# Optimization experiments

Measured on AMD Instinct MI355X. Metric: run time of the kernel, lower is better.

Reference implementation:

```python
import math
import jax, jax.numpy as jnp
import numpy as np

NUM_HEAD = 16

def get_slopes(n):
    def pow2(n):
        start = 2 ** (-(2 ** (-(math.log2(n) - 3))))
        return [start * start ** i for i in range(n)]
    if math.log2(n).is_integer():
        return pow2(n)
    c = 2 ** math.floor(math.log2(n))
    return pow2(c) + get_slopes(2 * c)[0::2][: n - c]

def setup_inputs() -> dict:
    key = jax.random.key(0)
    ks = jax.random.split(key, 5)
    B, T, D = 2, 2048, 1024
    x = jax.random.normal(ks[0], (B, T, D), dtype=jnp.float32)
    Wq = jax.random.normal(ks[1], (D, D), dtype=jnp.float32) * 0.02
    Wk = jax.random.normal(ks[2], (D, D), dtype=jnp.float32) * 0.02
    Wv = jax.random.normal(ks[3], (D, D), dtype=jnp.float32) * 0.02
    Wo = jax.random.normal(ks[4], (D, D), dtype=jnp.float32) * (0.02 / math.sqrt(2 * 24))
    return {"x": x, "Wq": Wq, "Wk": Wk, "Wv": Wv, "Wo": Wo}

def reference(x, Wq, Wk, Wv, Wo):
    B, T, D = x.shape
    H = NUM_HEAD
    hd = D // H
    # projections (no bias)
    q = (x @ Wq).reshape(B, T, H, hd).transpose(0, 2, 1, 3)  # b h t d
    k = (x @ Wk).reshape(B, T, H, hd).transpose(0, 2, 1, 3)
    v = (x @ Wv).reshape(B, T, H, hd).transpose(0, 2, 1, 3)
    scores = jnp.einsum("bhqd,bhkd->bhqk", q, k) / jnp.sqrt(jnp.asarray(hd, dtype=q.dtype))
    # ALiBi bias: slopes[h] * (j - (T-1)), broadcast over query positions
    slopes = jnp.asarray(np.array(get_slopes(H), dtype=np.float32))
    alibi = slopes[:, None, None] * (jnp.arange(T, dtype=jnp.float32) - (T - 1))[None, None, :]  # h 1 k
    scores = scores + alibi[None]  # b h q k
    causal = jnp.tril(jnp.ones((T, T), dtype=bool))
    masked = jnp.where(causal[None, None], scores.astype(jnp.float32), jnp.finfo(jnp.float32).min)
    p = jax.nn.softmax(masked, axis=-1)
    attn_out = jnp.einsum("bhqk,bhkd->bhqd", p, v)
    attn_out = attn_out.transpose(0, 2, 1, 3).reshape(B, T, D)
    return attn_out @ Wo
```

## Files before the change

kernel.cpp:

```cpp
#include <hip/hip_runtime.h>
#include <hip/hip_bf16.h>
#include <math.h>

#define B_ 2
#define T_ 2048
#define D_ 1024
#define H_ 16
#define HD 64

typedef __bf16 bf16;
typedef bf16 bf16x8 __attribute__((ext_vector_type(8)));
typedef bf16 bf16x4 __attribute__((ext_vector_type(4)));
typedef short short4v __attribute__((ext_vector_type(4)));
typedef float f32x4 __attribute__((ext_vector_type(4)));

#define GL2LDS16(g, l) __builtin_amdgcn_global_load_lds(                      \
    (const __attribute__((address_space(1))) void*)(g),                       \
    (__attribute__((address_space(3))) void*)(l), 16, 0, 0)

static __device__ __forceinline__ f32x4 mfma16x16x16(bf16x4 a, bf16x4 b, f32x4 c) {
#if defined(__HIP_DEVICE_COMPILE__)
# if __has_builtin(__builtin_amdgcn_mfma_f32_16x16x16bf16_1k)
    return __builtin_amdgcn_mfma_f32_16x16x16bf16_1k(
        __builtin_bit_cast(short4v, a), __builtin_bit_cast(short4v, b), c, 0, 0, 0);
# else
    asm("v_mfma_f32_16x16x16_bf16 %0, %1, %2, %0" : "+v"(c) : "v"(a), "v"(b));
    return c;
# endif
#else
    (void)a; (void)b;
    return c;
#endif
}

static __device__ __forceinline__ bf16x4 lo4(bf16x8 v) {
    return __builtin_shufflevector(v, v, 0, 1, 2, 3);
}
static __device__ __forceinline__ bf16x4 hi4(bf16x8 v) {
    return __builtin_shufflevector(v, v, 4, 5, 6, 7);
}

__global__ __launch_bounds__(256) void prep_inputs(const float* __restrict__ x,
                                                   const float* __restrict__ W0,
                                                   const float* __restrict__ W1,
                                                   const float* __restrict__ W2,
                                                   const float* __restrict__ W3,
                                                   bf16* __restrict__ xb,
                                                   bf16* __restrict__ Wt) {
    const int z = blockIdx.z;
    const int tid = threadIdx.x;
    if (z >= 4) {
        size_t i = ((((size_t)(z - 4) * 256 + blockIdx.y * 16 + blockIdx.x) * 256) + tid) * 4;
        float4 v = *(const float4*)(x + i);
        bf16 tmp[4] = {(bf16)v.x, (bf16)v.y, (bf16)v.z, (bf16)v.w};
        *(uint2*)(xb + i) = *(const uint2*)tmp;
        return;
    }
    __shared__ bf16 tile[64 * 72];
    const float* W = (z == 0) ? W0 : (z == 1) ? W1 : (z == 2) ? W2 : W3;
    bf16* out = Wt + (size_t)z * D_ * D_;
    const int k0 = blockIdx.y * 64, n0 = blockIdx.x * 64;
    for (int it = 0; it < 4; ++it) {
        int idx = it * 256 + tid;
        int r = idx >> 4;
        int c4 = (idx & 15) << 2;
        float4 v = *(const float4*)(W + (size_t)(k0 + r) * D_ + n0 + c4);
        tile[(c4 + 0) * 72 + r] = (bf16)v.x;
        tile[(c4 + 1) * 72 + r] = (bf16)v.y;
        tile[(c4 + 2) * 72 + r] = (bf16)v.z;
        tile[(c4 + 3) * 72 + r] = (bf16)v.w;
    }
    __syncthreads();
    for (int it = 0; it < 2; ++it) {
        int idx = it * 256 + tid;
        int r = idx >> 3;
        int c8 = (idx & 7) << 3;
        bf16x8 v = *(const bf16x8*)&tile[r * 72 + c8];
        *(bf16x8*)(out + (size_t)(n0 + r) * D_ + k0 + c8) = v;
    }
}

__global__ __launch_bounds__(256) void gemm_qkv(const bf16* __restrict__ A,
                                                const bf16* __restrict__ Bt,
                                                bf16* __restrict__ Cout) {
    __shared__ bf16 As[2][2][128 * 32];
    __shared__ bf16 Bs[2][3][2][64 * 32];
    const int bid = blockIdx.x;
    const int xcd = bid & 7, rr = bid >> 3;
    const int y   = (xcd << 2) + (rr & 3);
    const int xx  = rr >> 2;
    const int m0 = y * 128, n0 = xx * 64;

    const int tid = threadIdx.x;
    const int wave = tid >> 6, lane = tid & 63;
    const int quad = lane >> 4, l16 = lane & 15;
    const int wr = wave >> 1, wc = wave & 1;

    const int lrow = lane >> 2, lcol = (lane & 3) << 3;
    const bf16* ag = A + (size_t)(m0 + wave * 32 + lrow) * D_ + lcol;
    const size_t brow = (size_t)(n0 + wave * 16 + lrow) * D_ + lcol;
    const int a_off = (wave * 32 + lrow) * 32 + lcol;
    const int b_off = (wave * 16 + lrow) * 32 + lcol;

    f32x4 acc[3][4][2];
#pragma unroll
    for (int z = 0; z < 3; ++z)
#pragma unroll
        for (int mi = 0; mi < 4; ++mi)
#pragma unroll
            for (int ni = 0; ni < 2; ++ni) acc[z][mi][ni] = (f32x4){0.f, 0.f, 0.f, 0.f};

    auto stage = [&](int buf, int kb) {
        GL2LDS16(ag + kb,                        &As[buf][0][a_off]);
        GL2LDS16(ag + (size_t)16 * D_ + kb,      &As[buf][0][a_off + 16 * 32]);
        GL2LDS16(ag + kb + 32,                   &As[buf][1][a_off]);
        GL2LDS16(ag + (size_t)16 * D_ + kb + 32, &As[buf][1][a_off + 16 * 32]);
#pragma unroll
        for (int z = 0; z < 3; ++z) {
            const bf16* bg = Bt + (size_t)z * D_ * D_ + brow;
            GL2LDS16(bg + kb,      &Bs[buf][z][0][b_off]);
            GL2LDS16(bg + kb + 32, &Bs[buf][z][1][b_off]);
        }
    };

    stage(0, 0);
    __syncthreads();
    int cur = 0;
    for (int kb = 0; kb < D_; kb += 64) {
        if (kb + 64 < D_) stage(cur ^ 1, kb + 64);
#pragma unroll
        for (int half = 0; half < 2; ++half) {
            bf16x8 af[4];
#pragma unroll
            for (int mi = 0; mi < 4; ++mi)
                af[mi] = *(const bf16x8*)&As[cur][half][(wr * 64 + mi * 16 + l16) * 32 + quad * 8];
#pragma unroll
            for (int z = 0; z < 3; ++z) {
                bf16x8 bfr[2];
#pragma unroll
                for (int ni = 0; ni < 2; ++ni)
                    bfr[ni] = *(const bf16x8*)&Bs[cur][z][half][(wc * 32 + ni * 16 + l16) * 32 + quad * 8];
                if (z < 2) {
#pragma unroll
                    for (int mi = 0; mi < 4; ++mi)
#pragma unroll
                        for (int ni = 0; ni < 2; ++ni)
                            acc[z][mi][ni] = __builtin_amdgcn_mfma_f32_16x16x32_bf16(
                                bfr[ni], af[mi], acc[z][mi][ni], 0, 0, 0);
                } else {
#pragma unroll
                    for (int mi = 0; mi < 4; ++mi)
#pragma unroll
                        for (int ni = 0; ni < 2; ++ni)
                            acc[z][mi][ni] = __builtin_amdgcn_mfma_f32_16x16x32_bf16(
                                af[mi], bfr[ni], acc[z][mi][ni], 0, 0, 0);
                }
            }
        }
        __syncthreads();
        cur ^= 1;
    }

#pragma unroll
    for (int z = 0; z < 3; ++z) {
        bf16* Cb = Cout + (size_t)z * (B_ * T_) * D_;
        const float qscale = (z == 0) ? 0.180336887f : 1.0f;
        if (z < 2) {
#pragma unroll
            for (int mi = 0; mi < 4; ++mi)
#pragma unroll
                for (int ni = 0; ni < 2; ++ni) {
                    int m = m0 + wr * 64 + mi * 16 + l16;
                    int n = n0 + wc * 32 + ni * 16 + quad * 4;
                    int b = m >> 11, t = m & (T_ - 1);
                    int h = n >> 6, d = n & (HD - 1);
                    bf16 o4[4];
                    for (int r = 0; r < 4; ++r) o4[r] = (bf16)(acc[z][mi][ni][r] * qscale);
                    *(uint2*)&Cb[(((((size_t)b * H_ + h) * T_ + t) << 6) + d)] =
                        *(const uint2*)o4;
                }
        } else {
#pragma unroll
            for (int mi = 0; mi < 4; ++mi)
#pragma unroll
                for (int ni = 0; ni < 2; ++ni) {
                    int m = m0 + wr * 64 + mi * 16 + quad * 4;
                    int n = n0 + wc * 32 + ni * 16 + l16;
                    int b = m >> 11, t = m & (T_ - 1);
                    int h = n >> 6, d = n & (HD - 1);
                    bf16 o4[4];
                    for (int r = 0; r < 4; ++r) o4[r] = (bf16)acc[z][mi][ni][r];
                    *(uint2*)&Cb[((((size_t)b * H_ + h) * HD + d) * T_ + t)] =
                        *(const uint2*)o4;
                }
        }
    }
}

__global__ __launch_bounds__(256) void gemm_out(const bf16* __restrict__ A,
                                                const bf16* __restrict__ Bt,
                                                float* __restrict__ Cout) {
    __shared__ bf16 As[2][2][128 * 32];
    __shared__ bf16 Bs[2][2][64 * 32];
    const int bid = blockIdx.x;
    const int xcd = bid & 7, rr = bid >> 3;
    const int y   = (xcd << 2) + (rr & 3);
    const int xx  = rr >> 2;
    const int m0 = y * 128, n0 = xx * 64;

    const int tid = threadIdx.x;
    const int wave = tid >> 6, lane = tid & 63;
    const int quad = lane >> 4, l16 = lane & 15;
    const int wr = wave >> 1, wc = wave & 1;

    const int lrow = lane >> 2, lcol = (lane & 3) << 3;
    const bf16* ag = A  + (size_t)(m0 + wave * 32 + lrow) * D_ + lcol;
    const bf16* bg = Bt + (size_t)(n0 + wave * 16 + lrow) * D_ + lcol;
    const int a_off = (wave * 32 + lrow) * 32 + lcol;
    const int b_off = (wave * 16 + lrow) * 32 + lcol;

    f32x4 acc[4][2];
    for (int mi = 0; mi < 4; ++mi)
        for (int ni = 0; ni < 2; ++ni) acc[mi][ni] = (f32x4){0.f, 0.f, 0.f, 0.f};

    auto stage = [&](int buf, int kb) {
        GL2LDS16(ag + kb,                        &As[buf][0][a_off]);
        GL2LDS16(ag + (size_t)16 * D_ + kb,      &As[buf][0][a_off + 16 * 32]);
        GL2LDS16(ag + kb + 32,                   &As[buf][1][a_off]);
        GL2LDS16(ag + (size_t)16 * D_ + kb + 32, &As[buf][1][a_off + 16 * 32]);
        GL2LDS16(bg + kb,                        &Bs[buf][0][b_off]);
        GL2LDS16(bg + kb + 32,                   &Bs[buf][1][b_off]);
    };

    stage(0, 0);
    __syncthreads();
    int cur = 0;
    for (int kb = 0; kb < D_; kb += 64) {
        if (kb + 64 < D_) stage(cur ^ 1, kb + 64);
#pragma unroll
        for (int half = 0; half < 2; ++half) {
            bf16x8 af[4], bfr[2];
#pragma unroll
            for (int mi = 0; mi < 4; ++mi)
                af[mi] = *(const bf16x8*)&As[cur][half][(wr * 64 + mi * 16 + l16) * 32 + quad * 8];
#pragma unroll
            for (int ni = 0; ni < 2; ++ni)
                bfr[ni] = *(const bf16x8*)&Bs[cur][half][(wc * 32 + ni * 16 + l16) * 32 + quad * 8];
#pragma unroll
            for (int mi = 0; mi < 4; ++mi)
#pragma unroll
                for (int ni = 0; ni < 2; ++ni)
                    acc[mi][ni] = __builtin_amdgcn_mfma_f32_16x16x32_bf16(
                        bfr[ni], af[mi], acc[mi][ni], 0, 0, 0);
        }
        __syncthreads();
        cur ^= 1;
    }

    for (int mi = 0; mi < 4; ++mi)
        for (int ni = 0; ni < 2; ++ni) {
            int m = m0 + wr * 64 + mi * 16 + l16;
            int n = n0 + wc * 32 + ni * 16 + quad * 4;
            *(f32x4*)&Cout[(size_t)m * D_ + n] = acc[mi][ni];
        }
}

__device__ __constant__ unsigned char ITEM_QT[24] = {
    8,9,10,11,12,13,14,15, 7,15, 6,14, 5,13, 4,12, 3,11, 2,10, 1,9, 0,8};
__device__ __constant__ unsigned char ITEM_KIND[24] = {
    1,1,1,1,1,1,1,1, 0,2, 0,2, 0,2, 0,2, 0,2, 0,2, 0,2, 0,2};

#define LDP 136

struct VStage { bf16x8 v0, v1; };

__global__ __launch_bounds__(512, 4) void attn_kernel(const bf16* __restrict__ Q,
                                                      const bf16* __restrict__ K,
                                                      const bf16* __restrict__ Vt,
                                                      bf16* __restrict__ O,
                                                      float* __restrict__ Opart,
                                                      float2* __restrict__ ML) {
    __shared__ bf16 Kh[2][2][128 * 32];
    __shared__ bf16 Vs[64 * LDP];

    const int bh = blockIdx.x;
    const int item = blockIdx.y;
    const int qt = ITEM_QT[item];
    const int kind = ITEM_KIND[item];
    const int h = bh & (H_ - 1), b = bh >> 4;
    const int tid = threadIdx.x;
    const int wave = tid >> 6, lane = tid & 63;
    const int quad = lane >> 4, l16 = lane & 15;

    const bf16* Qb = Q + (size_t)bh * T_ * HD;
    const bf16* Kb = K + (size_t)bh * T_ * HD;
    const bf16* Vb = Vt + (size_t)bh * HD * T_;

    const float slope2 = exp2f(-0.5f * (float)(h + 1)) * 1.44269504f;

    bf16x8 qf[2];
    {
        const bf16* qrow = Qb + (size_t)(qt * 128 + wave * 16 + l16) * HD + quad * 8;
        qf[0] = *(const bf16x8*)(qrow);
        qf[1] = *(const bf16x8*)(qrow + 32);
    }

    auto stageK = [&](int buf, int t) {
        const bf16* kg = Kb + ((size_t)t * 128 + (tid >> 2)) * HD + ((tid & 3) << 3);
        GL2LDS16(kg,      &Kh[buf][0][tid * 8]);
        GL2LDS16(kg + 32, &Kh[buf][1][tid * 8]);
    };

    const int slot0 = tid, slot1 = 512 + tid;
    const int rv0 = slot0 >> 4, c0 = slot0 & 15;
    const int rv1 = slot1 >> 4, c1 = slot1 & 15;
    const int vs0 = rv0 * LDP + (c0 & 1) * 64 + (c0 >> 1) * 4;
    const int vs1 = rv1 * LDP + (c1 & 1) * 64 + (c1 >> 1) * 4;

    auto loadV = [&](int t, VStage& st) {
        const bf16* vb = Vb + t * 128;
        st.v0 = *(const bf16x8*)(vb + (size_t)rv0 * T_ + c0 * 8);
        st.v1 = *(const bf16x8*)(vb + (size_t)rv1 * T_ + c1 * 8);
    };
    auto storeV = [&](const VStage& st) {
        *(bf16x4*)&Vs[vs0]      = lo4(st.v0);
        *(bf16x4*)&Vs[vs0 + 32] = hi4(st.v0);
        *(bf16x4*)&Vs[vs1]      = lo4(st.v1);
        *(bf16x4*)&Vs[vs1 + 32] = hi4(st.v1);
    };

    f32x4 acc[4];
    for (int df = 0; df < 4; ++df) acc[df] = (f32x4){0.f, 0.f, 0.f, 0.f};
    float m_run = -INFINITY, l_lane = 0.f;

    const int qglob = qt * 128 + wave * 16 + l16;
    const int nkt = qt + 1;
    const int kt0 = (kind == 2) ? 8 : 0;
    const int kt1 = (kind == 1) ? 8 : nkt;

    auto compute = [&](int kt, int buf, bool last) {
        f32x4 s[8];
#pragma unroll
        for (int nf = 0; nf < 8; ++nf) {
            bf16x8 kf0 = *(const bf16x8*)&Kh[buf][0][(nf * 16 + l16) * 32 + quad * 8];
            bf16x8 kf1 = *(const bf16x8*)&Kh[buf][1][(nf * 16 + l16) * 32 + quad * 8];
            f32x4 zz = (f32x4){0.f, 0.f, 0.f, 0.f};
            __builtin_amdgcn_s_setprio(1);
            zz = __builtin_amdgcn_mfma_f32_16x16x32_bf16(kf0, qf[0], zz, 0, 0, 0);
            zz = __builtin_amdgcn_mfma_f32_16x16x32_bf16(kf1, qf[1], zz, 0, 0, 0);
            __builtin_amdgcn_s_setprio(0);
            s[nf] = zz;
        }

        const float j0f = (float)(kt * 128 + quad * 4 - (T_ - 1));
#pragma unroll
        for (int nf = 0; nf < 8; ++nf)
#pragma unroll
            for (int r = 0; r < 4; ++r)
                s[nf][r] += slope2 * (j0f + (float)(nf * 16 + r));
        if (last) {
            const int jb = kt * 128 + quad * 4;
#pragma unroll
            for (int nf = 0; nf < 8; ++nf)
#pragma unroll
                for (int r = 0; r < 4; ++r)
                    if (jb + nf * 16 + r > qglob) s[nf][r] = -INFINITY;
        }

        float a[8];
#pragma unroll
        for (int nf = 0; nf < 8; ++nf)
            a[nf] = fmaxf(fmaxf(s[nf][0], s[nf][1]), fmaxf(s[nf][2], s[nf][3]));
        float t0 = fmaxf(a[0], a[1]), t1 = fmaxf(a[2], a[3]);
        float t2 = fmaxf(a[4], a[5]), t3 = fmaxf(a[6], a[7]);
        float mx = fmaxf(fmaxf(t0, t1), fmaxf(t2, t3));
        mx = fmaxf(mx, __shfl_xor(mx, 16, 64));
        mx = fmaxf(mx, __shfl_xor(mx, 32, 64));

        if (!__all(mx - m_run <= 8.f)) {
            const float mnew = fmaxf(m_run, mx);
            const float alpha = exp2f(m_run - mnew);
            l_lane *= alpha;
#pragma unroll
            for (int df = 0; df < 4; ++df) acc[df] *= alpha;
            m_run = mnew;
        }

        float rs0 = 0.f, rs1 = 0.f;
        bf16x4 pf[8];
#pragma unroll
        for (int nf = 0; nf < 8; ++nf) {
            float p0 = exp2f(s[nf][0] - m_run);
            float p1 = exp2f(s[nf][1] - m_run);
            float p2 = exp2f(s[nf][2] - m_run);
            float p3 = exp2f(s[nf][3] - m_run);
            if (nf & 1) rs1 += (p0 + p1) + (p2 + p3);
            else        rs0 += (p0 + p1) + (p2 + p3);
            pf[nf] = (bf16x4){(bf16)p0, (bf16)p1, (bf16)p2, (bf16)p3};
        }
        l_lane += rs0 + rs1;

#pragma unroll
        for (int j = 0; j < 4; ++j) {
            bf16x8 w[4];
#pragma unroll
            for (int df = 0; df < 4; ++df)
                w[df] = *(const bf16x8*)&Vs[(df * 16 + l16) * LDP + quad * 32 + j * 8];
            __builtin_amdgcn_s_setprio(1);
#pragma unroll
            for (int df = 0; df < 4; ++df) {
                acc[df] = mfma16x16x16(lo4(w[df]), pf[2 * j],     acc[df]);
                acc[df] = mfma16x16x16(hi4(w[df]), pf[2 * j + 1], acc[df]);
            }
            __builtin_amdgcn_s_setprio(0);
        }
    };

    VStage sA, sB;
    stageK(0, kt0);
    loadV(kt0, sA);
    int kt = kt0;
    for (;;) {
        __syncthreads();
        storeV(sA);
        __syncthreads();
        if (kt + 1 < kt1) { stageK(1, kt + 1); loadV(kt + 1, sB); }
        compute(kt, 0, kt == nkt - 1);
        if (++kt >= kt1) break;
        __syncthreads();
        storeV(sB);
        __syncthreads();
        if (kt + 1 < kt1) { stageK(0, kt + 1); loadV(kt + 1, sA); }
        compute(kt, 1, kt == nkt - 1);
        if (++kt >= kt1) break;
    }

    float l_run = l_lane;
    l_run += __shfl_xor(l_run, 16, 64);
    l_run += __shfl_xor(l_run, 32, 64);

    if (kind == 0) {
        const float inv = 1.0f / l_run;
        for (int df = 0; df < 4; ++df) {
            bf16 o4[4];
            for (int r = 0; r < 4; ++r) o4[r] = (bf16)(acc[df][r] * inv);
            *(uint2*)&O[(((size_t)b * T_ + qglob) * H_ + h) * HD + df * 16 + quad * 4] =
                *(const uint2*)o4;
        }
    } else {
        const int pidx = (bh * 8 + (qt - 8)) * 2 + (kind == 2 ? 1 : 0);
        const int ql = wave * 16 + l16;
        float* dst = Opart + (size_t)pidx * 8192 + ql * 64;
        for (int df = 0; df < 4; ++df)
            *(f32x4*)&dst[df * 16 + quad * 4] = acc[df];
        if (quad == 0) ML[pidx * 128 + ql] = make_float2(m_run, l_run);
    }
}

__global__ __launch_bounds__(512) void attn_merge(const float* __restrict__ Opart,
                                                  const float2* __restrict__ ML,
                                                  bf16* __restrict__ O) {
    const int qt = 8 + blockIdx.x, bh = blockIdx.y;
    const int h = bh & (H_ - 1), b = bh >> 4;
    const int tid = threadIdx.x;
    const int q = tid >> 2, dc = (tid & 3) << 4;
    const int p0 = (bh * 8 + blockIdx.x) * 2, p1 = p0 + 1;

    const float2 ml0 = ML[p0 * 128 + q], ml1 = ML[p1 * 128 + q];
    const float M = fmaxf(ml0.x, ml1.x);
    const float e0 = exp2f(ml0.x - M), e1 = exp2f(ml1.x - M);
    const float inv = 1.0f / (e0 * ml0.y + e1 * ml1.y);

    const float* a = Opart + (size_t)p0 * 8192 + q * 64 + dc;
    const float* c = Opart + (size_t)p1 * 8192 + q * 64 + dc;
    bf16 o16[16];
    for (int j = 0; j < 4; ++j) {
        f32x4 va = *(const f32x4*)(a + j * 4);
        f32x4 vc = *(const f32x4*)(c + j * 4);
        for (int r = 0; r < 4; ++r)
            o16[j * 4 + r] = (bf16)((va[r] * e0 + vc[r] * e1) * inv);
    }
    const int t = qt * 128 + q;
    bf16* dst = O + (((size_t)b * T_ + t) * H_ + h) * HD + dc;
    *(bf16x8*)dst = *(const bf16x8*)o16;
    *(bf16x8*)(dst + 8) = *(const bf16x8*)(o16 + 8);
}

extern "C" void kernel_launch(void* const* d_in, const int* in_sizes, int n_in,
                              void* d_out, int out_size, void* d_ws, size_t ws_size,
                              hipStream_t stream) {
    const float* x  = (const float*)d_in[0];
    const float* Wq = (const float*)d_in[1];
    const float* Wk = (const float*)d_in[2];
    const float* Wv = (const float*)d_in[3];
    const float* Wo = (const float*)d_in[4];
    float* out = (float*)d_out;

    const size_t M = (size_t)B_ * T_;
    const size_t XE = M * D_;
    const size_t WE = (size_t)D_ * D_;

    char* ws = (char*)d_ws;
    size_t off = 0;
    auto carve = [&](size_t bytes) {
        void* p = ws + off;
        off += (bytes + 255) & ~(size_t)255;
        return p;
    };
    bf16* xb  = (bf16*)carve(XE * 2);
    bf16* Wt  = (bf16*)carve(4 * WE * 2);
    bf16* QKV = (bf16*)carve(3 * XE * 2);
    float*  Opart = (float*)carve(32 * 8 * 2 * 8192 * sizeof(float));
    float2* MLbuf = (float2*)carve(32 * 8 * 2 * 128 * sizeof(float2));
    bf16* attn = xb;

    prep_inputs<<<dim3(16, 16, 20), 256, 0, stream>>>(x, Wq, Wk, Wv, Wo, xb, Wt);

    gemm_qkv<<<512, 256, 0, stream>>>(xb, Wt, QKV);
    attn_kernel<<<dim3(32, 24), 512, 0, stream>>>(QKV, QKV + XE, QKV + 2 * XE,
                                                  attn, Opart, MLbuf);
    attn_merge<<<dim3(8, 32), 512, 0, stream>>>(Opart, MLbuf, attn);
    gemm_out<<<512, 256, 0, stream>>>(attn, Wt + 3 * WE, out);
}
```

Measured before the change: 182.8 us.

## Split causal attention into 4-tile KV chunks with multi-way partial merge

Replaces the two-way split of late query tiles with a finer split where each block handles at most four key tiles, giving 40 work items per head and a merge that combines up to four partials. This is meant to even out per-block work and raise parallelism in the attention kernel. K double buffering is removed, so K is now loaded synchronously each iteration, which shrinks shared memory but can expose load latency. Extra partial output writes and merge reads add memory traffic.

```diff
diff --git a/kernel.cpp b/kernel.cpp
--- a/kernel.cpp
+++ b/kernel.cpp
@@ -265,12 +265,18 @@
         }
 }
 
-__device__ __constant__ unsigned char ITEM_QT[24] = {
-    8,9,10,11,12,13,14,15, 7,15, 6,14, 5,13, 4,12, 3,11, 2,10, 1,9, 0,8};
-__device__ __constant__ unsigned char ITEM_KIND[24] = {
-    1,1,1,1,1,1,1,1, 0,2, 0,2, 0,2, 0,2, 0,2, 0,2, 0,2, 0,2};
+__device__ __constant__ unsigned char ITEM_QT[40] = {
+    15,15,15,15, 14,14,14, 13,13,13, 12,12,12, 11,11,11, 10,10, 9,9, 8,8, 7,7, 6, 5, 4, 3,
+    14,10,6,2, 13,9,5,1, 12,8,4,0};
+__device__ __constant__ unsigned char ITEM_C[40] = {
+    0,1,2,3, 0,1,2, 0,1,2, 0,1,2, 0,1,2, 0,1, 0,1, 0,1, 0,1, 0, 0, 0, 0,
+    3,2,1,0, 3,2,1,0, 3,2,1,0};
 
 #define LDP 136
+
+static __device__ __forceinline__ int psl_base(int qt) {
+    return (qt < 8) ? (qt - 4) * 2 : (qt < 12) ? 8 + (qt - 8) * 3 : 20 + (qt - 12) * 4;
+}
 
 struct VStage { bf16x8 v0, v1; };
 
@@ -280,13 +286,13 @@
                                                       bf16* __restrict__ O,
                                                       float* __restrict__ Opart,
                                                       float2* __restrict__ ML) {
-    __shared__ bf16 Kh[2][2][128 * 32];
+    __shared__ bf16 Kh[2][128 * 32];
     __shared__ bf16 Vs[64 * LDP];
 
     const int bh = blockIdx.x;
     const int item = blockIdx.y;
     const int qt = ITEM_QT[item];
-    const int kind = ITEM_KIND[item];
+    const int c  = ITEM_C[item];
     const int h = bh & (H_ - 1), b = bh >> 4;
     const int tid = threadIdx.x;
     const int wave = tid >> 6, lane = tid & 63;
@@ -305,10 +311,10 @@
         qf[1] = *(const bf16x8*)(qrow + 32);
     }
 
-    auto stageK = [&](int buf, int t) {
+    auto stageK = [&](int t) {
         const bf16* kg = Kb + ((size_t)t * 128 + (tid >> 2)) * HD + ((tid & 3) << 3);
-        GL2LDS16(kg,      &Kh[buf][0][tid * 8]);
-        GL2LDS16(kg + 32, &Kh[buf][1][tid * 8]);
+        GL2LDS16(kg,      &Kh[0][tid * 8]);
+        GL2LDS16(kg + 32, &Kh[1][tid * 8]);
     };
 
     const int slot0 = tid, slot1 = 512 + tid;
@@ -334,16 +340,15 @@
     float m_run = -INFINITY, l_lane = 0.f;
 
     const int qglob = qt * 128 + wave * 16 + l16;
-    const int nkt = qt + 1;
-    const int kt0 = (kind == 2) ? 8 : 0;
-    const int kt1 = (kind == 1) ? 8 : nkt;
-
-    auto compute = [&](int kt, int buf, bool last) {
+    const int kt0 = c * 4;
+    const int kt1 = min(kt0 + 4, qt + 1);
+
+    auto compute = [&](int kt, bool last) {
         f32x4 s[8];
 #pragma unroll
         for (int nf = 0; nf < 8; ++nf) {
-            bf16x8 kf0 = *(const bf16x8*)&Kh[buf][0][(nf * 16 + l16) * 32 + quad * 8];
-            bf16x8 kf1 = *(const bf16x8*)&Kh[buf][1][(nf * 16 + l16) * 32 + quad * 8];
+            bf16x8 kf0 = *(const bf16x8*)&Kh[0][(nf * 16 + l16) * 32 + quad * 8];
+            bf16x8 kf1 = *(const bf16x8*)&Kh[1][(nf * 16 + l16) * 32 + quad * 8];
             f32x4 zz = (f32x4){0.f, 0.f, 0.f, 0.f};
             __builtin_amdgcn_s_setprio(1);
             zz = __builtin_amdgcn_mfma_f32_16x16x32_bf16(kf0, qf[0], zz, 0, 0, 0);
@@ -417,21 +422,22 @@
     };
 
     VStage sA, sB;
-    stageK(0, kt0);
     loadV(kt0, sA);
     int kt = kt0;
     for (;;) {
         __syncthreads();
+        stageK(kt);
         storeV(sA);
         __syncthreads();
-        if (kt + 1 < kt1) { stageK(1, kt + 1); loadV(kt + 1, sB); }
-        compute(kt, 0, kt == nkt - 1);
+        if (kt + 1 < kt1) loadV(kt + 1, sB);
+        compute(kt, kt == qt);
         if (++kt >= kt1) break;
         __syncthreads();
+        stageK(kt);
         storeV(sB);
         __syncthreads();
-        if (kt + 1 < kt1) { stageK(0, kt + 1); loadV(kt + 1, sA); }
-        compute(kt, 1, kt == nkt - 1);
+        if (kt + 1 < kt1) loadV(kt + 1, sA);
+        compute(kt, kt == qt);
         if (++kt >= kt1) break;
     }
 
@@ -439,7 +445,7 @@
     l_run += __shfl_xor(l_run, 16, 64);
     l_run += __shfl_xor(l_run, 32, 64);
 
-    if (kind == 0) {
+    if (qt < 4) {
         const float inv = 1.0f / l_run;
         for (int df = 0; df < 4; ++df) {
             bf16 o4[4];
@@ -448,7 +454,7 @@
                 *(const uint2*)o4;
         }
     } else {
-        const int pidx = (bh * 8 + (qt - 8)) * 2 + (kind == 2 ? 1 : 0);
+        const int pidx = bh * 36 + psl_base(qt) + c;
         const int ql = wave * 16 + l16;
         float* dst = Opart + (size_t)pidx * 8192 + ql * 64;
         for (int df = 0; df < 4; ++df)
@@ -460,26 +466,44 @@
 __global__ __launch_bounds__(512) void attn_merge(const float* __restrict__ Opart,
                                                   const float2* __restrict__ ML,
                                                   bf16* __restrict__ O) {
-    const int qt = 8 + blockIdx.x, bh = blockIdx.y;
+    const int qt = 4 + blockIdx.x, bh = blockIdx.y;
+    const int C = (qt < 8) ? 2 : (qt < 12) ? 3 : 4;
+    const int p0 = bh * 36 + psl_base(qt);
     const int h = bh & (H_ - 1), b = bh >> 4;
     const int tid = threadIdx.x;
     const int q = tid >> 2, dc = (tid & 3) << 4;
-    const int p0 = (bh * 8 + blockIdx.x) * 2, p1 = p0 + 1;
-
-    const float2 ml0 = ML[p0 * 128 + q], ml1 = ML[p1 * 128 + q];
-    const float M = fmaxf(ml0.x, ml1.x);
-    const float e0 = exp2f(ml0.x - M), e1 = exp2f(ml1.x - M);
-    const float inv = 1.0f / (e0 * ml0.y + e1 * ml1.y);
-
-    const float* a = Opart + (size_t)p0 * 8192 + q * 64 + dc;
-    const float* c = Opart + (size_t)p1 * 8192 + q * 64 + dc;
+
+    float2 mls[4];
+#pragma unroll
+    for (int i = 0; i < 4; ++i)
+        mls[i] = (i < C) ? ML[(p0 + i) * 128 + q] : make_float2(-INFINITY, 0.f);
+    float M = fmaxf(fmaxf(mls[0].x, mls[1].x), fmaxf(mls[2].x, mls[3].x));
+    float e[4], lsum = 0.f;
+#pragma unroll
+    for (int i = 0; i < 4; ++i) { e[i] = exp2f(mls[i].x - M); lsum += e[i] * mls[i].y; }
+    const float inv = 1.0f / lsum;
+
+    f32x4 o[4];
+#pragma unroll
+    for (int j = 0; j < 4; ++j) o[j] = (f32x4){0.f, 0.f, 0.f, 0.f};
+#pragma unroll
+    for (int i = 0; i < 4; ++i) {
+        if (i < C) {
+            const float* pa = Opart + (size_t)(p0 + i) * 8192 + q * 64 + dc;
+#pragma unroll
+            for (int j = 0; j < 4; ++j) {
+                f32x4 va = *(const f32x4*)(pa + j * 4);
+#pragma unroll
+                for (int r = 0; r < 4; ++r) o[j][r] += va[r] * e[i];
+            }
+        }
+    }
+
     bf16 o16[16];
-    for (int j = 0; j < 4; ++j) {
-        f32x4 va = *(const f32x4*)(a + j * 4);
-        f32x4 vc = *(const f32x4*)(c + j * 4);
-        for (int r = 0; r < 4; ++r)
-            o16[j * 4 + r] = (bf16)((va[r] * e0 + vc[r] * e1) * inv);
-    }
+#pragma unroll
+    for (int j = 0; j < 4; ++j)
+#pragma unroll
+        for (int r = 0; r < 4; ++r) o16[j * 4 + r] = (bf16)(o[j][r] * inv);
     const int t = qt * 128 + q;
     bf16* dst = O + (((size_t)b * T_ + t) * H_ + h) * HD + dc;
     *(bf16x8*)dst = *(const bf16x8*)o16;
@@ -510,15 +534,15 @@
     bf16* xb  = (bf16*)carve(XE * 2);
     bf16* Wt  = (bf16*)carve(4 * WE * 2);
     bf16* QKV = (bf16*)carve(3 * XE * 2);
-    float*  Opart = (float*)carve(32 * 8 * 2 * 8192 * sizeof(float));
-    float2* MLbuf = (float2*)carve(32 * 8 * 2 * 128 * sizeof(float2));
+    float*  Opart = (float*)carve((size_t)32 * 36 * 8192 * sizeof(float));
+    float2* MLbuf = (float2*)carve((size_t)32 * 36 * 128 * sizeof(float2));
     bf16* attn = xb;
 
     prep_inputs<<<dim3(16, 16, 20), 256, 0, stream>>>(x, Wq, Wk, Wv, Wo, xb, Wt);
 
     gemm_qkv<<<512, 256, 0, stream>>>(xb, Wt, QKV);
-    attn_kernel<<<dim3(32, 24), 512, 0, stream>>>(QKV, QKV + XE, QKV + 2 * XE,
+    attn_kernel<<<dim3(32, 40), 512, 0, stream>>>(QKV, QKV + XE, QKV + 2 * XE,
                                                   attn, Opart, MLbuf);
-    attn_merge<<<dim3(8, 32), 512, 0, stream>>>(Opart, MLbuf, attn);
+    attn_merge<<<dim3(12, 32), 512, 0, stream>>>(Opart, MLbuf, attn);
     gemm_out<<<512, 256, 0, stream>>>(attn, Wt + 3 * WE, out);
 }
```

New measurement: 186.8 us. 1.02x slower.
